# Performance work log

Measured on AMD Instinct MI355X. Metric: run time of the kernel, lower is better.

## Reference

```python
import jax, jax.numpy as jnp
import numpy as np

# layer hyperparameters (init_kwargs)
SCORE_T = 0.05
IOU_T = 0.5
MAX_OUT = 300
BBOX_STD = np.array([0.1, 0.1, 0.2, 0.2], dtype=np.float32)


def setup_inputs() -> dict:
    key = jax.random.key(0)
    k1, k2, k3, k4 = jax.random.split(key, 4)
    B, N, C = 8, 2000, 81
    deltas = jax.random.normal(k1, (B, N, C, 4), jnp.float32) * 0.1
    class_logits = jax.random.normal(k2, (B, N, C), jnp.float32)
    # well-formed proposal boxes (y1,x1,y2,x2) in normalized coords + tag column
    cyx = jax.random.uniform(k3, (B, N, 2), jnp.float32, 0.1, 0.9)
    hw = jax.random.uniform(k4, (B, N, 2), jnp.float32, 0.05, 0.3)
    proposals = jnp.concatenate([cyx - hw * 0.5, cyx + hw * 0.5, jnp.ones((B, N, 1), jnp.float32)], axis=-1)
    return {"deltas": deltas, "class_logits": class_logits, "proposals": proposals}


def apply_regress(d, boxes):
    # d: [...,4] (dy,dx,dh,dw); boxes: [...,4] (y1,x1,y2,x2)
    h = boxes[..., 2] - boxes[..., 0]
    w = boxes[..., 3] - boxes[..., 1]
    cy = (boxes[..., 2] + boxes[..., 0]) * 0.5
    cx = (boxes[..., 3] + boxes[..., 1]) * 0.5
    d = d * jnp.asarray(BBOX_STD, d.dtype)
    cy = cy + d[..., 0] * h
    cx = cx + d[..., 1] * w
    h = h * jnp.exp(d[..., 2])
    w = w * jnp.exp(d[..., 3])
    return jnp.stack([cy - h * 0.5, cx - w * 0.5, cy + h * 0.5, cx + w * 0.5], axis=-1)


def box_iou(a, b):
    # a: [N,4], b: [M,4] -> [N,M]
    yx1 = jnp.maximum(a[:, None, :2], b[None, :, :2])
    yx2 = jnp.minimum(a[:, None, 2:], b[None, :, 2:])
    inter = jnp.prod(jnp.maximum(yx2 - yx1, 0.0), axis=-1)
    area_a = (a[:, 2] - a[:, 0]) * (a[:, 3] - a[:, 1])
    area_b = (b[:, 2] - b[:, 0]) * (b[:, 3] - b[:, 1])
    return inter / (area_a[:, None] + area_b[None, :] - inter + 1e-8)


def nms_one(boxes, scores, logits):
    # boxes [N,4], scores [N], logits [N,C]; greedy NMS, pad to MAX_OUT with tag column
    ious = box_iou(boxes, boxes)  # [N,N]
    live = jnp.where(scores > SCORE_T, scores, -1.0)

    def step(s, _):
        idx = jnp.argmax(s)
        ok = s[idx] > 0.0  # softmax scores are >0; -1.0 marks dead
        s = jnp.where(ious[idx] > IOU_T, -1.0, s)
        s = s.at[idx].set(-1.0)
        return s, (idx, ok)

    _, (idxs, oks) = jax.lax.scan(step, live, None, length=MAX_OUT)
    okf = oks.astype(boxes.dtype)[:, None]  # [MAX_OUT,1], 1=real box, 0=padding
    out_boxes = jnp.concatenate([boxes[idxs] * okf, okf], axis=-1)          # [MAX_OUT,5]
    out_scores = jnp.concatenate([scores[idxs][:, None] * okf, okf], axis=-1)  # [MAX_OUT,2]
    out_logits = logits[idxs] * okf                                          # [MAX_OUT,C]
    return out_boxes, out_scores, out_logits


def reference(deltas, class_logits, proposals):
    boxes_in = proposals[..., :-1]                         # drop tag -> [B,N,4]
    class_scores = jax.nn.softmax(class_logits, axis=-1)   # [B,N,C]
    fg_scores = jnp.max(class_scores[..., 1:], axis=-1)    # [B,N]
    fg_cls = jnp.argmax(class_scores[..., 1:], axis=-1) + 1  # [B,N] best fg class
    # select class-specific delta for the best foreground class
    sel_deltas = jnp.take_along_axis(deltas, fg_cls[..., None, None], axis=2)[..., 0, :]  # [B,N,4]
    detect_boxes = apply_regress(sel_deltas, boxes_in)      # [B,N,4]
    return jax.vmap(nms_one)(detect_boxes, fg_scores, class_logits)
```

## Files before the change

kernel.cpp:

```cpp
#include <hip/hip_runtime.h>

#define BATCH 8
#define NBOX 2000
#define NCLS 81
#define NPAD 2048
#define MAX_OUT 300
#define SCORE_T 0.05f
#define IOU_T 0.5f
#define MASK_WORDS 64
#define WDEPTH 64

#define WS_BOXES   0
#define WS_SCORES  256000
#define WS_SKEY    320000
#define WS_SBOX    451072
#define WS_LARR    713216
#define WS_KLIST   713248
#define WS_KCOUNT  722848
#define WS_MASK    786432

__global__ void prep_kernel(const float* __restrict__ deltas,
                            const float* __restrict__ logits,
                            const float* __restrict__ proposals,
                            float4* __restrict__ boxes_out,
                            float* __restrict__ scores_out,
                            int* __restrict__ Larr) {
    int bn = blockIdx.x * blockDim.x + threadIdx.x;
    if (bn < BATCH) Larr[bn] = 0;
    if (bn >= BATCH * NBOX) return;

    const float* l = logits + (long)bn * NCLS;

    float M = l[0];
    #pragma unroll 4
    for (int c = 1; c < NCLS; ++c) M = fmaxf(M, l[c]);

    float S = 0.0f;
    float bl = -3.0e38f; int bc = 1;
    #pragma unroll 4
    for (int c = 0; c < NCLS; ++c) {
        float v = l[c];
        S += expf(v - M);
        if (c >= 1 && v > bl) { bl = v; bc = c; }
    }
    float score = expf(bl - M) / S;

    const float* p = proposals + (long)bn * 5;
    float y1 = p[0], x1 = p[1], y2 = p[2], x2 = p[3];
    float h = y2 - y1, w = x2 - x1;
    float cy = (y2 + y1) * 0.5f, cx = (x2 + x1) * 0.5f;

    const float* d = deltas + ((long)bn * NCLS + bc) * 4;
    float d0 = d[0] * 0.1f, d1 = d[1] * 0.1f, d2 = d[2] * 0.2f, d3 = d[3] * 0.2f;

    cy = cy + d0 * h;
    cx = cx + d1 * w;
    h = h * expf(d2);
    w = w * expf(d3);

    boxes_out[bn] = make_float4(cy - h * 0.5f, cx - w * 0.5f,
                                cy + h * 0.5f, cx + w * 0.5f);
    scores_out[bn] = score;
}

__global__ __launch_bounds__(512) void rank_kernel(
        const float* __restrict__ scores,
        const float4* __restrict__ boxes,
        unsigned long long* __restrict__ skey,
        float4* __restrict__ sbox,
        int* __restrict__ Larr) {
    int bid = blockIdx.x;
    int b = bid & 7, rb = bid >> 3;
    int t = threadIdx.x;

    __shared__ unsigned long long s_key[NPAD + 16];
    __shared__ int s_part[64][8];

    for (int c = t; c < NPAD; c += 512) {
        unsigned int bits = 0u;
        if (c < NBOX) bits = __float_as_uint(scores[b * NBOX + c]);
        s_key[c + (c >> 7)] =
            ((unsigned long long)bits << 32) |
            (unsigned long long)(0xFFFFFFFFu - (unsigned)c);
    }
    __syncthreads();

    int own = rb * 64 + (t >> 3);
    int seg = t & 7;
    unsigned long long mykey = s_key[own + (own >> 7)];
    int cnt = 0;
    int cbase = seg * 256;
    #pragma unroll 4
    for (int j = 0; j < 256; ++j) {
        int c = cbase + j;
        cnt += (s_key[c + (c >> 7)] > mykey) ? 1 : 0;
    }
    s_part[t >> 3][seg] = cnt;
    __syncthreads();

    if (t < 64) {
        int own2 = rb * 64 + t;
        unsigned long long key = s_key[own2 + (own2 >> 7)];
        int rank = s_part[t][0] + s_part[t][1] + s_part[t][2] + s_part[t][3]
                 + s_part[t][4] + s_part[t][5] + s_part[t][6] + s_part[t][7];
        skey[b * NPAD + rank] = key;
        unsigned int orig = 0xFFFFFFFFu - (unsigned int)key;
        float4 bx = make_float4(0.f, 0.f, 0.f, 0.f);
        if (orig < NBOX) bx = boxes[b * NBOX + orig];
        sbox[b * NPAD + rank] = bx;
        float sc = __uint_as_float((unsigned int)(key >> 32));
        if (sc > SCORE_T) atomicMax(&Larr[b], rank + 1);
    }
}

__global__ __launch_bounds__(512) void mask_kernel(
        const float4* __restrict__ sbox,
        const int* __restrict__ Larr,
        unsigned int* __restrict__ mask) {
    int bid = blockIdx.x;
    int b = bid & 7, rb = bid >> 3;
    int L = Larr[b];
    if (rb * 64 >= L) return;
    int t = threadIdx.x;

    __shared__ float4 s_bx[NPAD + 16];

    for (int c = t; c < NPAD; c += 512)
        s_bx[c + (c >> 7)] = sbox[b * NPAD + c];
    __syncthreads();

    int r   = rb * 64 + (t & 63);
    int seg = t >> 6;
    float4 rbx = s_bx[r + (r >> 7)];
    float rar = (rbx.z - rbx.x) * (rbx.w - rbx.y);
    unsigned int* outp = mask + (((size_t)(b * NPAD + r)) << 6);

    for (int w = 0; w < 8; ++w) {
        int wi = (seg << 3) + w;
        unsigned int bits = 0u;
        int colbase = wi << 5;
        if (colbase + 31 > r && colbase < L) {
            #pragma unroll 8
            for (int c2 = 0; c2 < 32; ++c2) {
                int col = colbase + c2;
                float4 ob = s_bx[col + (col >> 7)];
                float oa = (ob.z - ob.x) * (ob.w - ob.y);
                float yy1 = fmaxf(rbx.x, ob.x), xx1 = fmaxf(rbx.y, ob.y);
                float yy2 = fminf(rbx.z, ob.z), xx2 = fminf(rbx.w, ob.w);
                float inter = fmaxf(yy2 - yy1, 0.f) * fmaxf(xx2 - xx1, 0.f);
                float iou = inter / (rar + oa - inter + 1e-8f);
                bits |= (iou > IOU_T) ? (1u << c2) : 0u;
            }
        }
        outp[wi] = bits;
    }
}

__global__ __launch_bounds__(64) void walk_kernel(
        const int* __restrict__ Larr,
        const unsigned int* __restrict__ mask,
        int* __restrict__ klist,
        int* __restrict__ kcount) {
    int b = blockIdx.x;
    int lane = threadIdx.x;

    __shared__ int s_cand[WDEPTH];
    __shared__ unsigned int s_clrw[64];
    __shared__ int s_kl[MAX_OUT];

    int L = Larr[b];
    int nset = L - (lane << 5);
    nset = nset < 0 ? 0 : (nset > 32 ? 32 : nset);
    unsigned int alive = (nset >= 32) ? 0xFFFFFFFFu
                        : ((nset <= 0) ? 0u : ((1u << nset) - 1u));

    const unsigned int* M = mask + ((size_t)b * NPAD) * MASK_WORDS;
    int kept = 0;

    while (kept < MAX_OUT) {
        unsigned long long ne = __ballot(alive != 0u);
        if (!ne) break;

        int mypc = __builtin_popcount(alive);
        int incl = mypc;
        #pragma unroll
        for (int off = 1; off < 64; off <<= 1) {
            int n = __shfl_up(incl, off);
            if (lane >= off) incl += n;
        }
        int excl = incl - mypc;
        int total = __builtin_amdgcn_readlane(incl, 63);
        int ncand = total < WDEPTH ? total : WDEPTH;

        {
            unsigned int aw = alive;
            int pos = excl;
            while (aw && pos < WDEPTH) {
                int bit = (int)__builtin_ctz(aw);
                aw &= aw - 1u;
                s_cand[pos] = (lane << 5) + bit;
                pos++;
            }
        }
        __syncthreads();

        int candv = s_cand[lane < ncand ? lane : 0];

        int cdsc[WDEPTH];
        #pragma unroll
        for (int d = 0; d < WDEPTH; ++d)
            cdsc[d] = __builtin_amdgcn_readlane(candv, d);

        unsigned int rowA[WDEPTH];
        #pragma unroll
        for (int d = 0; d < WDEPTH; ++d)
            rowA[d] = M[((size_t)cdsc[d] << 6) + lane];

        unsigned int colw[WDEPTH];
        int myw = candv >> 5;
        #pragma unroll
        for (int e = 0; e < WDEPTH; ++e)
            colw[e] = M[((size_t)cdsc[e] << 6) + myw];

        int sh = candv & 31;
        unsigned int colv_lo = 0u, colv_hi = 0u;
        #pragma unroll
        for (int e = 0; e < 32; ++e)
            colv_lo |= ((colw[e] >> sh) & 1u) << e;
        #pragma unroll
        for (int e = 32; e < WDEPTH; ++e)
            colv_hi |= ((colw[e] >> sh) & 1u) << (e - 32);

        unsigned long long sub[WDEPTH];
        #pragma unroll
        for (int e = 0; e < 32; ++e)
            sub[e] = __ballot(((colv_lo >> e) & 1u) != 0u);
        #pragma unroll
        for (int e = 32; e < WDEPTH; ++e)
            sub[e] = __ballot(((colv_hi >> (e - 32)) & 1u) != 0u);

        unsigned long long live =
            (ncand >= 64) ? ~0ull : ((1ull << ncand) - 1ull);
        unsigned long long committed = 0ull;
        int kept_base = kept;
        #pragma unroll
        for (int e = 0; e < WDEPTH; ++e) {
            if (kept < MAX_OUT && ((live >> e) & 1ull)) {
                committed |= 1ull << e;
                kept++;
                live &= ~sub[e];
            }
        }

        unsigned int acc = 0u;
        #pragma unroll
        for (int d = 0; d < WDEPTH; ++d) {
            unsigned int m = 0u - (unsigned int)((committed >> d) & 1ull);
            acc |= rowA[d] & m;
        }
        alive &= ~acc;

        s_clrw[lane] = 0u;
        __syncthreads();
        if (lane < ncand && ((committed >> lane) & 1ull))
            atomicOr(&s_clrw[candv >> 5], 1u << (candv & 31));
        __syncthreads();
        alive &= ~s_clrw[lane];

        if (lane < ncand && ((committed >> lane) & 1ull)) {
            int pos = kept_base +
                (int)__builtin_popcountll(committed & ((1ull << lane) - 1ull));
            s_kl[pos] = candv;
        }
        __syncthreads();
    }

    if (lane == 0) kcount[b] = kept;
    __syncthreads();
    for (int k = lane; k < kept; k += 64)
        klist[b * MAX_OUT + k] = s_kl[k];
}

__global__ void out_kernel(const unsigned long long* __restrict__ skey,
                           const float4* __restrict__ sbox,
                           const int* __restrict__ klist,
                           const int* __restrict__ kcount,
                           const float* __restrict__ logits,
                           float* __restrict__ out) {
    int idx = blockIdx.x * blockDim.x + threadIdx.x;
    const int NB = BATCH * MAX_OUT * 5;
    const int NS = BATCH * MAX_OUT * 2;
    const int NL = BATCH * MAX_OUT * NCLS;
    if (idx >= NB + NS + NL) return;

    if (idx < NB) {
        int b = idx / (MAX_OUT * 5);
        int rem = idx - b * (MAX_OUT * 5);
        int k = rem / 5, c = rem - 5 * k;
        float v = 0.f;
        if (k < kcount[b]) {
            if (c == 4) v = 1.f;
            else {
                float4 bx = sbox[b * NPAD + klist[b * MAX_OUT + k]];
                v = (c == 0) ? bx.x : (c == 1) ? bx.y : (c == 2) ? bx.z : bx.w;
            }
        }
        out[idx] = v;
    } else if (idx < NB + NS) {
        int j = idx - NB;
        int b = j / (MAX_OUT * 2);
        int rem = j - b * (MAX_OUT * 2);
        int k = rem >> 1, c = rem & 1;
        float v = 0.f;
        if (k < kcount[b]) {
            if (c) v = 1.f;
            else {
                unsigned long long key = skey[b * NPAD + klist[b * MAX_OUT + k]];
                v = __uint_as_float((unsigned int)(key >> 32));
            }
        }
        out[idx] = v;
    } else {
        int j = idx - NB - NS;
        int b = j / (MAX_OUT * NCLS);
        int rem = j - b * (MAX_OUT * NCLS);
        int k = rem / NCLS, c = rem - NCLS * k;
        float v = 0.f;
        if (k < kcount[b]) {
            unsigned long long key = skey[b * NPAD + klist[b * MAX_OUT + k]];
            unsigned int orig = 0xFFFFFFFFu - (unsigned int)key;
            v = logits[((long)b * NBOX + orig) * NCLS + c];
        }
        out[idx] = v;
    }
}

extern "C" void kernel_launch(void* const* d_in, const int* in_sizes, int n_in,
                              void* d_out, int out_size, void* d_ws, size_t ws_size,
                              hipStream_t stream) {
    const float* deltas    = (const float*)d_in[0];
    const float* logits    = (const float*)d_in[1];
    const float* proposals = (const float*)d_in[2];
    float* out = (float*)d_out;

    char* ws = (char*)d_ws;
    float4* ws_boxes  = (float4*)(ws + WS_BOXES);
    float*  ws_scores = (float*)(ws + WS_SCORES);
    unsigned long long* ws_skey = (unsigned long long*)(ws + WS_SKEY);
    float4* ws_sbox   = (float4*)(ws + WS_SBOX);
    int*    ws_Larr   = (int*)(ws + WS_LARR);
    int*    ws_klist  = (int*)(ws + WS_KLIST);
    int*    ws_kcount = (int*)(ws + WS_KCOUNT);
    unsigned int* ws_mask = (unsigned int*)(ws + WS_MASK);

    prep_kernel<<<(BATCH * NBOX + 255) / 256, 256, 0, stream>>>(
        deltas, logits, proposals, ws_boxes, ws_scores, ws_Larr);
    rank_kernel<<<BATCH * (NPAD / 64), 512, 0, stream>>>(
        ws_scores, ws_boxes, ws_skey, ws_sbox, ws_Larr);
    mask_kernel<<<BATCH * (NPAD / 64), 512, 0, stream>>>(
        ws_sbox, ws_Larr, ws_mask);
    walk_kernel<<<BATCH, 64, 0, stream>>>(
        ws_Larr, ws_mask, ws_klist, ws_kcount);
    int total_out = BATCH * MAX_OUT * (5 + 2 + NCLS);
    out_kernel<<<(total_out + 255) / 256, 256, 0, stream>>>(
        ws_skey, ws_sbox, ws_klist, ws_kcount, logits, out);
}
```

Measured before the change: 108.2 us.

## Fuse all NMS stages into one cooperative kernel with grid syncs

Replaces the five separate launches (prep, rank, mask, walk, output) with a single cooperative kernel of 256 blocks that separates the phases with grid.sync. The prep phase now spreads each box's softmax over 8 lanes, using shuffle reductions for the max, the sum and the argmax. The walk phase drops the shared-memory clear-word atomics and block barriers, ballots the column bits directly, and writes the keep list straight to global memory. The aim is to remove per-launch gaps and speed up the logits pass, at the cost of grid-wide barriers and a co-residency requirement for the cooperative launch.

```diff
diff --git a/kernel.cpp b/kernel.cpp
--- a/kernel.cpp
+++ b/kernel.cpp
@@ -1,4 +1,7 @@
 #include <hip/hip_runtime.h>
+#include <hip/hip_cooperative_groups.h>
+
+namespace cg = cooperative_groups;
 
 #define BATCH 8
 #define NBOX 2000
@@ -9,6 +12,8 @@
 #define IOU_T 0.5f
 #define MASK_WORDS 64
 #define WDEPTH 64
+#define NBLK 256
+#define NTHR 512
 
 #define WS_BOXES   0
 #define WS_SCORES  256000
@@ -19,319 +24,300 @@
 #define WS_KCOUNT  722848
 #define WS_MASK    786432
 
-__global__ void prep_kernel(const float* __restrict__ deltas,
-                            const float* __restrict__ logits,
-                            const float* __restrict__ proposals,
-                            float4* __restrict__ boxes_out,
-                            float* __restrict__ scores_out,
-                            int* __restrict__ Larr) {
-    int bn = blockIdx.x * blockDim.x + threadIdx.x;
-    if (bn < BATCH) Larr[bn] = 0;
-    if (bn >= BATCH * NBOX) return;
-
-    const float* l = logits + (long)bn * NCLS;
-
-    float M = l[0];
-    #pragma unroll 4
-    for (int c = 1; c < NCLS; ++c) M = fmaxf(M, l[c]);
-
-    float S = 0.0f;
-    float bl = -3.0e38f; int bc = 1;
-    #pragma unroll 4
-    for (int c = 0; c < NCLS; ++c) {
-        float v = l[c];
-        S += expf(v - M);
-        if (c >= 1 && v > bl) { bl = v; bc = c; }
-    }
-    float score = expf(bl - M) / S;
-
-    const float* p = proposals + (long)bn * 5;
-    float y1 = p[0], x1 = p[1], y2 = p[2], x2 = p[3];
-    float h = y2 - y1, w = x2 - x1;
-    float cy = (y2 + y1) * 0.5f, cx = (x2 + x1) * 0.5f;
-
-    const float* d = deltas + ((long)bn * NCLS + bc) * 4;
-    float d0 = d[0] * 0.1f, d1 = d[1] * 0.1f, d2 = d[2] * 0.2f, d3 = d[3] * 0.2f;
-
-    cy = cy + d0 * h;
-    cx = cx + d1 * w;
-    h = h * expf(d2);
-    w = w * expf(d3);
-
-    boxes_out[bn] = make_float4(cy - h * 0.5f, cx - w * 0.5f,
-                                cy + h * 0.5f, cx + w * 0.5f);
-    scores_out[bn] = score;
-}
-
-__global__ __launch_bounds__(512) void rank_kernel(
-        const float* __restrict__ scores,
-        const float4* __restrict__ boxes,
+__global__ __launch_bounds__(NTHR) void mega_kernel(
+        const float* __restrict__ deltas,
+        const float* __restrict__ logits,
+        const float* __restrict__ proposals,
+        float4* __restrict__ boxes,
+        float* __restrict__ scores,
         unsigned long long* __restrict__ skey,
         float4* __restrict__ sbox,
-        int* __restrict__ Larr) {
+        int* __restrict__ Larr,
+        int* __restrict__ klist,
+        int* __restrict__ kcount,
+        unsigned int* __restrict__ mask,
+        float* __restrict__ out) {
+    cg::grid_group grid = cg::this_grid();
     int bid = blockIdx.x;
-    int b = bid & 7, rb = bid >> 3;
     int t = threadIdx.x;
-
-    __shared__ unsigned long long s_key[NPAD + 16];
-    __shared__ int s_part[64][8];
-
-    for (int c = t; c < NPAD; c += 512) {
-        unsigned int bits = 0u;
-        if (c < NBOX) bits = __float_as_uint(scores[b * NBOX + c]);
-        s_key[c + (c >> 7)] =
-            ((unsigned long long)bits << 32) |
-            (unsigned long long)(0xFFFFFFFFu - (unsigned)c);
-    }
-    __syncthreads();
-
-    int own = rb * 64 + (t >> 3);
-    int seg = t & 7;
-    unsigned long long mykey = s_key[own + (own >> 7)];
-    int cnt = 0;
-    int cbase = seg * 256;
-    #pragma unroll 4
-    for (int j = 0; j < 256; ++j) {
-        int c = cbase + j;
-        cnt += (s_key[c + (c >> 7)] > mykey) ? 1 : 0;
-    }
-    s_part[t >> 3][seg] = cnt;
-    __syncthreads();
-
-    if (t < 64) {
-        int own2 = rb * 64 + t;
-        unsigned long long key = s_key[own2 + (own2 >> 7)];
-        int rank = s_part[t][0] + s_part[t][1] + s_part[t][2] + s_part[t][3]
-                 + s_part[t][4] + s_part[t][5] + s_part[t][6] + s_part[t][7];
-        skey[b * NPAD + rank] = key;
-        unsigned int orig = 0xFFFFFFFFu - (unsigned int)key;
-        float4 bx = make_float4(0.f, 0.f, 0.f, 0.f);
-        if (orig < NBOX) bx = boxes[b * NBOX + orig];
-        sbox[b * NPAD + rank] = bx;
-        float sc = __uint_as_float((unsigned int)(key >> 32));
-        if (sc > SCORE_T) atomicMax(&Larr[b], rank + 1);
-    }
-}
-
-__global__ __launch_bounds__(512) void mask_kernel(
-        const float4* __restrict__ sbox,
-        const int* __restrict__ Larr,
-        unsigned int* __restrict__ mask) {
-    int bid = blockIdx.x;
-    int b = bid & 7, rb = bid >> 3;
-    int L = Larr[b];
-    if (rb * 64 >= L) return;
-    int t = threadIdx.x;
-
-    __shared__ float4 s_bx[NPAD + 16];
-
-    for (int c = t; c < NPAD; c += 512)
-        s_bx[c + (c >> 7)] = sbox[b * NPAD + c];
-    __syncthreads();
-
-    int r   = rb * 64 + (t & 63);
-    int seg = t >> 6;
-    float4 rbx = s_bx[r + (r >> 7)];
-    float rar = (rbx.z - rbx.x) * (rbx.w - rbx.y);
-    unsigned int* outp = mask + (((size_t)(b * NPAD + r)) << 6);
-
-    for (int w = 0; w < 8; ++w) {
-        int wi = (seg << 3) + w;
-        unsigned int bits = 0u;
-        int colbase = wi << 5;
-        if (colbase + 31 > r && colbase < L) {
-            #pragma unroll 8
-            for (int c2 = 0; c2 < 32; ++c2) {
-                int col = colbase + c2;
-                float4 ob = s_bx[col + (col >> 7)];
-                float oa = (ob.z - ob.x) * (ob.w - ob.y);
-                float yy1 = fmaxf(rbx.x, ob.x), xx1 = fmaxf(rbx.y, ob.y);
-                float yy2 = fminf(rbx.z, ob.z), xx2 = fminf(rbx.w, ob.w);
-                float inter = fmaxf(yy2 - yy1, 0.f) * fmaxf(xx2 - xx1, 0.f);
-                float iou = inter / (rar + oa - inter + 1e-8f);
-                bits |= (iou > IOU_T) ? (1u << c2) : 0u;
-            }
-        }
-        outp[wi] = bits;
-    }
-}
-
-__global__ __launch_bounds__(64) void walk_kernel(
-        const int* __restrict__ Larr,
-        const unsigned int* __restrict__ mask,
-        int* __restrict__ klist,
-        int* __restrict__ kcount) {
-    int b = blockIdx.x;
-    int lane = threadIdx.x;
-
-    __shared__ int s_cand[WDEPTH];
-    __shared__ unsigned int s_clrw[64];
-    __shared__ int s_kl[MAX_OUT];
-
-    int L = Larr[b];
-    int nset = L - (lane << 5);
-    nset = nset < 0 ? 0 : (nset > 32 ? 32 : nset);
-    unsigned int alive = (nset >= 32) ? 0xFFFFFFFFu
-                        : ((nset <= 0) ? 0u : ((1u << nset) - 1u));
-
-    const unsigned int* M = mask + ((size_t)b * NPAD) * MASK_WORDS;
-    int kept = 0;
-
-    while (kept < MAX_OUT) {
-        unsigned long long ne = __ballot(alive != 0u);
-        if (!ne) break;
-
-        int mypc = __builtin_popcount(alive);
-        int incl = mypc;
-        #pragma unroll
-        for (int off = 1; off < 64; off <<= 1) {
-            int n = __shfl_up(incl, off);
-            if (lane >= off) incl += n;
-        }
-        int excl = incl - mypc;
-        int total = __builtin_amdgcn_readlane(incl, 63);
-        int ncand = total < WDEPTH ? total : WDEPTH;
-
-        {
-            unsigned int aw = alive;
-            int pos = excl;
-            while (aw && pos < WDEPTH) {
-                int bit = (int)__builtin_ctz(aw);
-                aw &= aw - 1u;
-                s_cand[pos] = (lane << 5) + bit;
-                pos++;
-            }
+    int gtid = bid * NTHR + t;
+
+    __shared__ __align__(16) char smem[(NPAD + 16) * 16];
+
+    {
+        if (gtid < BATCH) Larr[gtid] = 0;
+        int g = gtid >> 3;
+        int j = t & 7;
+        if (g < BATCH * NBOX) {
+            const float* l = logits + (long)g * NCLS;
+            float M = -3.0e38f;
+            float bl = -3.0e38f; int bc = 0;
+            for (int c = j; c < NCLS; c += 8) {
+                float v = l[c];
+                M = fmaxf(M, v);
+                if (c >= 1 && v > bl) { bl = v; bc = c; }
+            }
+            #pragma unroll
+            for (int off = 1; off < 8; off <<= 1)
+                M = fmaxf(M, __shfl_xor(M, off));
+            float S = 0.f;
+            for (int c = j; c < NCLS; c += 8) S += expf(l[c] - M);
+            #pragma unroll
+            for (int off = 1; off < 8; off <<= 1) S += __shfl_xor(S, off);
+            #pragma unroll
+            for (int off = 1; off < 8; off <<= 1) {
+                float ov = __shfl_xor(bl, off);
+                int   oi = __shfl_xor(bc, off);
+                if (ov > bl || (ov == bl && oi < bc)) { bl = ov; bc = oi; }
+            }
+            if (j == 0) {
+                float score = expf(bl - M) / S;
+                const float* p = proposals + (long)g * 5;
+                float y1 = p[0], x1 = p[1], y2 = p[2], x2 = p[3];
+                float h = y2 - y1, w = x2 - x1;
+                float cy = (y2 + y1) * 0.5f, cx = (x2 + x1) * 0.5f;
+                const float* dd = deltas + ((long)g * NCLS + bc) * 4;
+                float d0 = dd[0] * 0.1f, d1 = dd[1] * 0.1f;
+                float d2 = dd[2] * 0.2f, d3 = dd[3] * 0.2f;
+                cy = cy + d0 * h;
+                cx = cx + d1 * w;
+                h = h * expf(d2);
+                w = w * expf(d3);
+                boxes[g] = make_float4(cy - h * 0.5f, cx - w * 0.5f,
+                                       cy + h * 0.5f, cx + w * 0.5f);
+                scores[g] = score;
+            }
+        }
+    }
+    grid.sync();
+
+    {
+        unsigned long long* s_key = (unsigned long long*)smem;
+        int (*s_part)[8] = (int(*)[8])(void*)(smem + (NPAD + 16) * 8);
+        int b = bid & 7, rb = bid >> 3;
+
+        for (int c = t; c < NPAD; c += NTHR) {
+            unsigned int bits = 0u;
+            if (c < NBOX) bits = __float_as_uint(scores[b * NBOX + c]);
+            s_key[c + (c >> 7)] =
+                ((unsigned long long)bits << 32) |
+                (unsigned long long)(0xFFFFFFFFu - (unsigned)c);
         }
         __syncthreads();
 
-        int candv = s_cand[lane < ncand ? lane : 0];
-
-        int cdsc[WDEPTH];
-        #pragma unroll
-        for (int d = 0; d < WDEPTH; ++d)
-            cdsc[d] = __builtin_amdgcn_readlane(candv, d);
-
-        unsigned int rowA[WDEPTH];
-        #pragma unroll
-        for (int d = 0; d < WDEPTH; ++d)
-            rowA[d] = M[((size_t)cdsc[d] << 6) + lane];
-
-        unsigned int colw[WDEPTH];
-        int myw = candv >> 5;
-        #pragma unroll
-        for (int e = 0; e < WDEPTH; ++e)
-            colw[e] = M[((size_t)cdsc[e] << 6) + myw];
-
-        int sh = candv & 31;
-        unsigned int colv_lo = 0u, colv_hi = 0u;
-        #pragma unroll
-        for (int e = 0; e < 32; ++e)
-            colv_lo |= ((colw[e] >> sh) & 1u) << e;
-        #pragma unroll
-        for (int e = 32; e < WDEPTH; ++e)
-            colv_hi |= ((colw[e] >> sh) & 1u) << (e - 32);
-
-        unsigned long long sub[WDEPTH];
-        #pragma unroll
-        for (int e = 0; e < 32; ++e)
-            sub[e] = __ballot(((colv_lo >> e) & 1u) != 0u);
-        #pragma unroll
-        for (int e = 32; e < WDEPTH; ++e)
-            sub[e] = __ballot(((colv_hi >> (e - 32)) & 1u) != 0u);
-
-        unsigned long long live =
-            (ncand >= 64) ? ~0ull : ((1ull << ncand) - 1ull);
-        unsigned long long committed = 0ull;
-        int kept_base = kept;
-        #pragma unroll
-        for (int e = 0; e < WDEPTH; ++e) {
-            if (kept < MAX_OUT && ((live >> e) & 1ull)) {
-                committed |= 1ull << e;
-                kept++;
-                live &= ~sub[e];
-            }
-        }
-
-        unsigned int acc = 0u;
-        #pragma unroll
-        for (int d = 0; d < WDEPTH; ++d) {
-            unsigned int m = 0u - (unsigned int)((committed >> d) & 1ull);
-            acc |= rowA[d] & m;
-        }
-        alive &= ~acc;
-
-        s_clrw[lane] = 0u;
+        int own = rb * 64 + (t >> 3);
+        int seg = t & 7;
+        unsigned long long mykey = s_key[own + (own >> 7)];
+        int cnt = 0;
+        int cbase = seg * 256;
+        #pragma unroll 4
+        for (int jj = 0; jj < 256; ++jj) {
+            int c = cbase + jj;
+            cnt += (s_key[c + (c >> 7)] > mykey) ? 1 : 0;
+        }
+        s_part[t >> 3][seg] = cnt;
         __syncthreads();
-        if (lane < ncand && ((committed >> lane) & 1ull))
-            atomicOr(&s_clrw[candv >> 5], 1u << (candv & 31));
-        __syncthreads();
-        alive &= ~s_clrw[lane];
-
-        if (lane < ncand && ((committed >> lane) & 1ull)) {
-            int pos = kept_base +
-                (int)__builtin_popcountll(committed & ((1ull << lane) - 1ull));
-            s_kl[pos] = candv;
-        }
-        __syncthreads();
-    }
-
-    if (lane == 0) kcount[b] = kept;
-    __syncthreads();
-    for (int k = lane; k < kept; k += 64)
-        klist[b * MAX_OUT + k] = s_kl[k];
-}
-
-__global__ void out_kernel(const unsigned long long* __restrict__ skey,
-                           const float4* __restrict__ sbox,
-                           const int* __restrict__ klist,
-                           const int* __restrict__ kcount,
-                           const float* __restrict__ logits,
-                           float* __restrict__ out) {
-    int idx = blockIdx.x * blockDim.x + threadIdx.x;
-    const int NB = BATCH * MAX_OUT * 5;
-    const int NS = BATCH * MAX_OUT * 2;
-    const int NL = BATCH * MAX_OUT * NCLS;
-    if (idx >= NB + NS + NL) return;
-
-    if (idx < NB) {
-        int b = idx / (MAX_OUT * 5);
-        int rem = idx - b * (MAX_OUT * 5);
-        int k = rem / 5, c = rem - 5 * k;
-        float v = 0.f;
-        if (k < kcount[b]) {
-            if (c == 4) v = 1.f;
-            else {
-                float4 bx = sbox[b * NPAD + klist[b * MAX_OUT + k]];
-                v = (c == 0) ? bx.x : (c == 1) ? bx.y : (c == 2) ? bx.z : bx.w;
-            }
-        }
-        out[idx] = v;
-    } else if (idx < NB + NS) {
-        int j = idx - NB;
-        int b = j / (MAX_OUT * 2);
-        int rem = j - b * (MAX_OUT * 2);
-        int k = rem >> 1, c = rem & 1;
-        float v = 0.f;
-        if (k < kcount[b]) {
-            if (c) v = 1.f;
-            else {
-                unsigned long long key = skey[b * NPAD + klist[b * MAX_OUT + k]];
-                v = __uint_as_float((unsigned int)(key >> 32));
-            }
-        }
-        out[idx] = v;
-    } else {
-        int j = idx - NB - NS;
-        int b = j / (MAX_OUT * NCLS);
-        int rem = j - b * (MAX_OUT * NCLS);
-        int k = rem / NCLS, c = rem - NCLS * k;
-        float v = 0.f;
-        if (k < kcount[b]) {
-            unsigned long long key = skey[b * NPAD + klist[b * MAX_OUT + k]];
+
+        if (t < 64) {
+            int own2 = rb * 64 + t;
+            unsigned long long key = s_key[own2 + (own2 >> 7)];
+            int rank = s_part[t][0] + s_part[t][1] + s_part[t][2] + s_part[t][3]
+                     + s_part[t][4] + s_part[t][5] + s_part[t][6] + s_part[t][7];
+            skey[b * NPAD + rank] = key;
             unsigned int orig = 0xFFFFFFFFu - (unsigned int)key;
-            v = logits[((long)b * NBOX + orig) * NCLS + c];
-        }
-        out[idx] = v;
+            float4 bx = make_float4(0.f, 0.f, 0.f, 0.f);
+            if (orig < NBOX) bx = boxes[b * NBOX + orig];
+            sbox[b * NPAD + rank] = bx;
+            float sc = __uint_as_float((unsigned int)(key >> 32));
+            if (sc > SCORE_T) atomicMax(&Larr[b], rank + 1);
+        }
+    }
+    grid.sync();
+
+    {
+        int b = bid & 7, rb = bid >> 3;
+        int L = Larr[b];
+        if (rb * 64 < L) {
+            float4* s_bx = (float4*)smem;
+            for (int c = t; c < NPAD; c += NTHR)
+                s_bx[c + (c >> 7)] = sbox[b * NPAD + c];
+            __syncthreads();
+
+            int r   = rb * 64 + (t & 63);
+            int seg = t >> 6;
+            float4 rbx = s_bx[r + (r >> 7)];
+            float rar = (rbx.z - rbx.x) * (rbx.w - rbx.y);
+            unsigned int* outp = mask + (((size_t)(b * NPAD + r)) << 6);
+
+            for (int w = 0; w < 8; ++w) {
+                int wi = (seg << 3) + w;
+                unsigned int bits = 0u;
+                int colbase = wi << 5;
+                if (colbase + 31 > r && colbase < L) {
+                    #pragma unroll 8
+                    for (int c2 = 0; c2 < 32; ++c2) {
+                        int col = colbase + c2;
+                        float4 ob = s_bx[col + (col >> 7)];
+                        float oa = (ob.z - ob.x) * (ob.w - ob.y);
+                        float yy1 = fmaxf(rbx.x, ob.x), xx1 = fmaxf(rbx.y, ob.y);
+                        float yy2 = fminf(rbx.z, ob.z), xx2 = fminf(rbx.w, ob.w);
+                        float inter = fmaxf(yy2 - yy1, 0.f) * fmaxf(xx2 - xx1, 0.f);
+                        float iou = inter / (rar + oa - inter + 1e-8f);
+                        bits |= (iou > IOU_T) ? (1u << c2) : 0u;
+                    }
+                }
+                outp[wi] = bits;
+            }
+        }
+    }
+    grid.sync();
+
+    if (bid < BATCH && t < 64) {
+        int b = bid;
+        int lane = t;
+        int* s_cand = (int*)smem;
+
+        int L = Larr[b];
+        int nset = L - (lane << 5);
+        nset = nset < 0 ? 0 : (nset > 32 ? 32 : nset);
+        unsigned int alive = (nset >= 32) ? 0xFFFFFFFFu
+                            : ((nset <= 0) ? 0u : ((1u << nset) - 1u));
+
+        const unsigned int* M = mask + ((size_t)b * NPAD) * MASK_WORDS;
+        int kept = 0;
+
+        while (kept < MAX_OUT) {
+            unsigned long long ne = __ballot(alive != 0u);
+            if (!ne) break;
+
+            int mypc = __builtin_popcount(alive);
+            int incl = mypc;
+            #pragma unroll
+            for (int off = 1; off < 64; off <<= 1) {
+                int n = __shfl_up(incl, off);
+                if (lane >= off) incl += n;
+            }
+            int excl = incl - mypc;
+            int total = __builtin_amdgcn_readlane(incl, 63);
+            int ncand = total < WDEPTH ? total : WDEPTH;
+
+            {
+                unsigned int aw = alive;
+                int pos = excl;
+                while (aw && pos < WDEPTH) {
+                    int bit = (int)__builtin_ctz(aw);
+                    aw &= aw - 1u;
+                    s_cand[pos] = (lane << 5) + bit;
+                    pos++;
+                }
+            }
+            asm volatile("s_waitcnt lgkmcnt(0)" ::: "memory");
+
+            int candv = s_cand[lane < ncand ? lane : 0];
+
+            int cdsc[WDEPTH];
+            #pragma unroll
+            for (int d = 0; d < WDEPTH; ++d)
+                cdsc[d] = __builtin_amdgcn_readlane(candv, d);
+
+            unsigned int rowA[WDEPTH];
+            #pragma unroll
+            for (int d = 0; d < WDEPTH; ++d)
+                rowA[d] = M[((size_t)cdsc[d] << 6) + lane];
+
+            int myw = candv >> 5;
+            int sh = candv & 31;
+            unsigned int colw[WDEPTH];
+            #pragma unroll
+            for (int e = 0; e < WDEPTH; ++e)
+                colw[e] = M[((size_t)cdsc[e] << 6) + myw];
+
+            unsigned long long sub[WDEPTH];
+            #pragma unroll
+            for (int e = 0; e < WDEPTH; ++e)
+                sub[e] = __ballot(((colw[e] >> sh) & 1u) != 0u);
+
+            unsigned long long live =
+                (ncand >= 64) ? ~0ull : ((1ull << ncand) - 1ull);
+            unsigned long long committed = 0ull;
+            int kept_base = kept;
+            #pragma unroll
+            for (int e = 0; e < WDEPTH; ++e) {
+                if (kept < MAX_OUT && ((live >> e) & 1ull)) {
+                    committed |= 1ull << e;
+                    kept++;
+                    live &= ~sub[e];
+                }
+            }
+
+            unsigned int acc = 0u;
+            #pragma unroll
+            for (int d = 0; d < WDEPTH; ++d) {
+                unsigned int m = 0u - (unsigned int)((committed >> d) & 1ull);
+                acc |= rowA[d] & m;
+            }
+            alive &= ~acc;
+
+            #pragma unroll
+            for (int d = 0; d < WDEPTH; ++d) {
+                if ((committed >> d) & 1ull) {
+                    if (lane == (cdsc[d] >> 5))
+                        alive &= ~(1u << (cdsc[d] & 31));
+                }
+            }
+
+            if (lane < ncand && ((committed >> lane) & 1ull)) {
+                int pos = kept_base +
+                    (int)__builtin_popcountll(committed & ((1ull << lane) - 1ull));
+                klist[b * MAX_OUT + pos] = candv;
+            }
+        }
+        if (lane == 0) kcount[b] = kept;
+    }
+    grid.sync();
+
+    {
+        const int NB = BATCH * MAX_OUT * 5;
+        const int NS = BATCH * MAX_OUT * 2;
+        const int NL = BATCH * MAX_OUT * NCLS;
+        const int TOT = NB + NS + NL;
+        for (int idx = gtid; idx < TOT; idx += NBLK * NTHR) {
+            float v = 0.f;
+            if (idx < NB) {
+                int b = idx / (MAX_OUT * 5);
+                int rem = idx - b * (MAX_OUT * 5);
+                int k = rem / 5, c = rem - 5 * k;
+                if (k < kcount[b]) {
+                    if (c == 4) v = 1.f;
+                    else {
+                        float4 bx = sbox[b * NPAD + klist[b * MAX_OUT + k]];
+                        v = (c == 0) ? bx.x : (c == 1) ? bx.y
+                          : (c == 2) ? bx.z : bx.w;
+                    }
+                }
+            } else if (idx < NB + NS) {
+                int jj = idx - NB;
+                int b = jj / (MAX_OUT * 2);
+                int rem = jj - b * (MAX_OUT * 2);
+                int k = rem >> 1, c = rem & 1;
+                if (k < kcount[b]) {
+                    if (c) v = 1.f;
+                    else v = __uint_as_float((unsigned int)
+                             (skey[b * NPAD + klist[b * MAX_OUT + k]] >> 32));
+                }
+            } else {
+                int jj = idx - NB - NS;
+                int b = jj / (MAX_OUT * NCLS);
+                int rem = jj - b * (MAX_OUT * NCLS);
+                int k = rem / NCLS, c = rem - NCLS * k;
+                if (k < kcount[b]) {
+                    unsigned long long key = skey[b * NPAD + klist[b * MAX_OUT + k]];
+                    unsigned int orig = 0xFFFFFFFFu - (unsigned int)key;
+                    v = logits[((long)b * NBOX + orig) * NCLS + c];
+                }
+            }
+            out[idx] = v;
+        }
     }
 }
 
@@ -353,15 +339,12 @@
     int*    ws_kcount = (int*)(ws + WS_KCOUNT);
     unsigned int* ws_mask = (unsigned int*)(ws + WS_MASK);
 
-    prep_kernel<<<(BATCH * NBOX + 255) / 256, 256, 0, stream>>>(
-        deltas, logits, proposals, ws_boxes, ws_scores, ws_Larr);
-    rank_kernel<<<BATCH * (NPAD / 64), 512, 0, stream>>>(
-        ws_scores, ws_boxes, ws_skey, ws_sbox, ws_Larr);
-    mask_kernel<<<BATCH * (NPAD / 64), 512, 0, stream>>>(
-        ws_sbox, ws_Larr, ws_mask);
-    walk_kernel<<<BATCH, 64, 0, stream>>>(
-        ws_Larr, ws_mask, ws_klist, ws_kcount);
-    int total_out = BATCH * MAX_OUT * (5 + 2 + NCLS);
-    out_kernel<<<(total_out + 255) / 256, 256, 0, stream>>>(
-        ws_skey, ws_sbox, ws_klist, ws_kcount, logits, out);
+    void* args[] = {
+        (void*)&deltas, (void*)&logits, (void*)&proposals,
+        (void*)&ws_boxes, (void*)&ws_scores, (void*)&ws_skey,
+        (void*)&ws_sbox, (void*)&ws_Larr, (void*)&ws_klist,
+        (void*)&ws_kcount, (void*)&ws_mask, (void*)&out
+    };
+    hipLaunchCooperativeKernel((void*)mega_kernel, dim3(NBLK), dim3(NTHR),
+                               args, 0, stream);
 }
```

New measurement: 211.5 us. 1.95x slower.

## Split softmax rows across 8 lanes and drop LDS syncs in NMS walk

Applied to the files above, without the earlier changes.

The prep kernel now gives each box's 81-class softmax/argmax to 8 lanes and combines the partial results with xor shuffles, where before one thread looped over the whole row serially. The walk kernel takes the candidate column words from the already loaded rowA via __shfl instead of issuing a second set of 64 global loads. It also clears committed bits with register logic instead of LDS atomics, writes klist directly to global memory, and replaces the barriers with an lgkmcnt wait, which relies on the block being a single wavefront. The costs are 8x more threads in prep and a per-candidate shuffle loop in the walk.

```diff
diff --git a/kernel.cpp b/kernel.cpp
--- a/kernel.cpp
+++ b/kernel.cpp
@@ -19,48 +19,57 @@
 #define WS_KCOUNT  722848
 #define WS_MASK    786432
 
-__global__ void prep_kernel(const float* __restrict__ deltas,
-                            const float* __restrict__ logits,
-                            const float* __restrict__ proposals,
-                            float4* __restrict__ boxes_out,
-                            float* __restrict__ scores_out,
-                            int* __restrict__ Larr) {
-    int bn = blockIdx.x * blockDim.x + threadIdx.x;
-    if (bn < BATCH) Larr[bn] = 0;
-    if (bn >= BATCH * NBOX) return;
-
-    const float* l = logits + (long)bn * NCLS;
-
-    float M = l[0];
-    #pragma unroll 4
-    for (int c = 1; c < NCLS; ++c) M = fmaxf(M, l[c]);
-
-    float S = 0.0f;
-    float bl = -3.0e38f; int bc = 1;
-    #pragma unroll 4
-    for (int c = 0; c < NCLS; ++c) {
+__global__ __launch_bounds__(256) void prep_kernel(
+        const float* __restrict__ deltas,
+        const float* __restrict__ logits,
+        const float* __restrict__ proposals,
+        float4* __restrict__ boxes_out,
+        float* __restrict__ scores_out,
+        int* __restrict__ Larr) {
+    int gtid = blockIdx.x * 256 + threadIdx.x;
+    if (gtid < BATCH) Larr[gtid] = 0;
+    int g = gtid >> 3;
+    int j = threadIdx.x & 7;
+    if (g >= BATCH * NBOX) return;
+
+    const float* l = logits + (long)g * NCLS;
+    float M = -3.0e38f;
+    float bl = -3.0e38f; int bc = 0;
+    for (int c = j; c < NCLS; c += 8) {
         float v = l[c];
-        S += expf(v - M);
+        M = fmaxf(M, v);
         if (c >= 1 && v > bl) { bl = v; bc = c; }
     }
-    float score = expf(bl - M) / S;
-
-    const float* p = proposals + (long)bn * 5;
-    float y1 = p[0], x1 = p[1], y2 = p[2], x2 = p[3];
-    float h = y2 - y1, w = x2 - x1;
-    float cy = (y2 + y1) * 0.5f, cx = (x2 + x1) * 0.5f;
-
-    const float* d = deltas + ((long)bn * NCLS + bc) * 4;
-    float d0 = d[0] * 0.1f, d1 = d[1] * 0.1f, d2 = d[2] * 0.2f, d3 = d[3] * 0.2f;
-
-    cy = cy + d0 * h;
-    cx = cx + d1 * w;
-    h = h * expf(d2);
-    w = w * expf(d3);
-
-    boxes_out[bn] = make_float4(cy - h * 0.5f, cx - w * 0.5f,
-                                cy + h * 0.5f, cx + w * 0.5f);
-    scores_out[bn] = score;
+    #pragma unroll
+    for (int off = 1; off < 8; off <<= 1)
+        M = fmaxf(M, __shfl_xor(M, off));
+    float S = 0.f;
+    for (int c = j; c < NCLS; c += 8) S += expf(l[c] - M);
+    #pragma unroll
+    for (int off = 1; off < 8; off <<= 1) S += __shfl_xor(S, off);
+    #pragma unroll
+    for (int off = 1; off < 8; off <<= 1) {
+        float ov = __shfl_xor(bl, off);
+        int   oi = __shfl_xor(bc, off);
+        if (ov > bl || (ov == bl && oi < bc)) { bl = ov; bc = oi; }
+    }
+    if (j == 0) {
+        float score = expf(bl - M) / S;
+        const float* p = proposals + (long)g * 5;
+        float y1 = p[0], x1 = p[1], y2 = p[2], x2 = p[3];
+        float h = y2 - y1, w = x2 - x1;
+        float cy = (y2 + y1) * 0.5f, cx = (x2 + x1) * 0.5f;
+        const float* dd = deltas + ((long)g * NCLS + bc) * 4;
+        float d0 = dd[0] * 0.1f, d1 = dd[1] * 0.1f;
+        float d2 = dd[2] * 0.2f, d3 = dd[3] * 0.2f;
+        cy = cy + d0 * h;
+        cx = cx + d1 * w;
+        h = h * expf(d2);
+        w = w * expf(d3);
+        boxes_out[g] = make_float4(cy - h * 0.5f, cx - w * 0.5f,
+                                   cy + h * 0.5f, cx + w * 0.5f);
+        scores_out[g] = score;
+    }
 }
 
 __global__ __launch_bounds__(512) void rank_kernel(
@@ -91,8 +100,8 @@
     int cnt = 0;
     int cbase = seg * 256;
     #pragma unroll 4
-    for (int j = 0; j < 256; ++j) {
-        int c = cbase + j;
+    for (int jj = 0; jj < 256; ++jj) {
+        int c = cbase + jj;
         cnt += (s_key[c + (c >> 7)] > mykey) ? 1 : 0;
     }
     s_part[t >> 3][seg] = cnt;
@@ -165,8 +174,6 @@
     int lane = threadIdx.x;
 
     __shared__ int s_cand[WDEPTH];
-    __shared__ unsigned int s_clrw[64];
-    __shared__ int s_kl[MAX_OUT];
 
     int L = Larr[b];
     int nset = L - (lane << 5);
@@ -202,7 +209,7 @@
                 pos++;
             }
         }
-        __syncthreads();
+        asm volatile("s_waitcnt lgkmcnt(0)" ::: "memory");
 
         int candv = s_cand[lane < ncand ? lane : 0];
 
@@ -216,28 +223,15 @@
         for (int d = 0; d < WDEPTH; ++d)
             rowA[d] = M[((size_t)cdsc[d] << 6) + lane];
 
-        unsigned int colw[WDEPTH];
         int myw = candv >> 5;
-        #pragma unroll
-        for (int e = 0; e < WDEPTH; ++e)
-            colw[e] = M[((size_t)cdsc[e] << 6) + myw];
-
         int sh = candv & 31;
-        unsigned int colv_lo = 0u, colv_hi = 0u;
-        #pragma unroll
-        for (int e = 0; e < 32; ++e)
-            colv_lo |= ((colw[e] >> sh) & 1u) << e;
-        #pragma unroll
-        for (int e = 32; e < WDEPTH; ++e)
-            colv_hi |= ((colw[e] >> sh) & 1u) << (e - 32);
 
         unsigned long long sub[WDEPTH];
         #pragma unroll
-        for (int e = 0; e < 32; ++e)
-            sub[e] = __ballot(((colv_lo >> e) & 1u) != 0u);
-        #pragma unroll
-        for (int e = 32; e < WDEPTH; ++e)
-            sub[e] = __ballot(((colv_hi >> (e - 32)) & 1u) != 0u);
+        for (int e = 0; e < WDEPTH; ++e) {
+            unsigned int cw = (unsigned int)__shfl((int)rowA[e], myw);
+            sub[e] = __ballot(((cw >> sh) & 1u) != 0u);
+        }
 
         unsigned long long live =
             (ncand >= 64) ? ~0ull : ((1ull << ncand) - 1ull);
@@ -260,25 +254,21 @@
         }
         alive &= ~acc;
 
-        s_clrw[lane] = 0u;
-        __syncthreads();
-        if (lane < ncand && ((committed >> lane) & 1ull))
-            atomicOr(&s_clrw[candv >> 5], 1u << (candv & 31));
-        __syncthreads();
-        alive &= ~s_clrw[lane];
+        #pragma unroll
+        for (int d = 0; d < WDEPTH; ++d) {
+            if ((committed >> d) & 1ull) {
+                if (lane == (cdsc[d] >> 5))
+                    alive &= ~(1u << (cdsc[d] & 31));
+            }
+        }
 
         if (lane < ncand && ((committed >> lane) & 1ull)) {
             int pos = kept_base +
                 (int)__builtin_popcountll(committed & ((1ull << lane) - 1ull));
-            s_kl[pos] = candv;
-        }
-        __syncthreads();
-    }
-
+            klist[b * MAX_OUT + pos] = candv;
+        }
+    }
     if (lane == 0) kcount[b] = kept;
-    __syncthreads();
-    for (int k = lane; k < kept; k += 64)
-        klist[b * MAX_OUT + k] = s_kl[k];
 }
 
 __global__ void out_kernel(const unsigned long long* __restrict__ skey,
@@ -353,7 +343,7 @@
     int*    ws_kcount = (int*)(ws + WS_KCOUNT);
     unsigned int* ws_mask = (unsigned int*)(ws + WS_MASK);
 
-    prep_kernel<<<(BATCH * NBOX + 255) / 256, 256, 0, stream>>>(
+    prep_kernel<<<(BATCH * NBOX * 8 + 255) / 256, 256, 0, stream>>>(
         deltas, logits, proposals, ws_boxes, ws_scores, ws_Larr);
     rank_kernel<<<BATCH * (NPAD / 64), 512, 0, stream>>>(
         ws_scores, ws_boxes, ws_skey, ws_sbox, ws_Larr);
```

After: 125.6 us. 1.16x slower.
